# Optimization experiments

Measured on AMD Instinct MI355X. Metric: run time of the kernel, lower is better.

## Reference

```python
import jax, jax.numpy as jnp
import numpy as np

PAST = 12
FUTURE = 12


def setup_inputs() -> dict:
    key = jax.random.key(0)
    k1, k2, k3, k4, k5 = jax.random.split(key, 5)
    B, L, D = 64, 256, 512
    inp = jax.random.normal(k1, (B, L, D), dtype=jnp.float32)
    W_t = jax.random.normal(k2, (FUTURE, PAST), dtype=jnp.float32) / np.sqrt(PAST)
    b_t = jax.random.normal(k3, (FUTURE,), dtype=jnp.float32) * 0.01
    W_s = jax.random.normal(k4, (D, D), dtype=jnp.float32) / np.sqrt(D)
    b_s = jax.random.normal(k5, (D,), dtype=jnp.float32) * 0.01
    return {"inp": inp, "W_t": W_t, "b_t": b_t, "W_s": W_s, "b_s": b_s}


def reference(inp, W_t, b_t, W_s, b_s):
    # inp: [B, L, D]. Sliding windows of size PAST -> W = L - PAST windows.
    B, L, D = inp.shape
    W = L - PAST
    # gather windows: [B, W, PAST, D]
    idx = jnp.arange(W)[:, None] + jnp.arange(PAST)[None, :]  # [W, PAST]
    x_win = inp[:, idx, :]  # [B, W, PAST, D]
    # temporal Linear(PAST -> FUTURE) along window-time axis
    t = jnp.einsum('bwpd,fp->bwfd', x_win, W_t) + b_t[None, None, :, None]
    # spatial Linear(D -> D) along last axis
    out = jnp.einsum('bwfd,ed->bwfe', t, W_s) + b_s
    return out  # [B, W, FUTURE, D]
```

## Files before the change

kernel.cpp:

```cpp
#include <hip/hip_runtime.h>

#define PAST 12
#define FUTURE 12
#define NB 64
#define NL 256
#define ND 512
#define NW 244

typedef unsigned short ushort_t;
typedef __attribute__((ext_vector_type(8))) short short8;
typedef __attribute__((ext_vector_type(4))) float floatx4;

__device__ inline unsigned int f2bf(float x) {
    unsigned int u = __float_as_uint(x);
    return (u + 0x7fffu + ((u >> 16) & 1u)) >> 16;
}

__global__ __launch_bounds__(256) void prep_ws(
    const float* __restrict__ Ws, ushort_t* __restrict__ Wsb, float* __restrict__ S)
{
    const int row = blockIdx.x;
    const int t = threadIdx.x;
    const float2 v = *(const float2*)(Ws + (size_t)row * ND + t * 2);
    *(unsigned int*)(Wsb + (size_t)row * ND + t * 2) = f2bf(v.x) | (f2bf(v.y) << 16);
    float s = v.x + v.y;
#pragma unroll
    for (int o = 32; o > 0; o >>= 1) s += __shfl_down(s, o);
    __shared__ float red[4];
    if ((t & 63) == 0) red[t >> 6] = s;
    __syncthreads();
    if (t == 0) S[row] = red[0] + red[1] + red[2] + red[3];
}

#define BM 128
#define BN 128
#define BK 32

#define STAGE_A_LOAD(k0) do { \
    _Pragma("unroll") \
    for (int c = 0; c < 4; ++c) av[c] = *(const float4*)(aptr[c] + (k0)); \
} while (0)

#define STAGE_A_WRITE(dst) do { \
    _Pragma("unroll") \
    for (int c = 0; c < 4; ++c) { \
        uint2 o; \
        o.x = f2bf(av[c].x) | (f2bf(av[c].y) << 16); \
        o.y = f2bf(av[c].z) | (f2bf(av[c].w) << 16); \
        *(uint2*)((dst) + tid * 4 + c * 1024) = o; \
    } \
} while (0)

#define STAGE_B(k0, dst) do { \
    _Pragma("unroll") \
    for (int r = 0; r < 2; ++r) { \
        const ushort_t* gb = Bm + (size_t)(n0 + (tid >> 2) + r * 64) * ND + (k0) + (tid & 3) * 8; \
        __builtin_amdgcn_global_load_lds( \
            (const __attribute__((address_space(1))) unsigned int*)gb, \
            (__attribute__((address_space(3))) unsigned int*)((dst) + r * 2048 + tid * 8), \
            16, 0, 0); \
    } \
} while (0)

#define GEMM_STEP(cura, curb) do { \
    const ushort_t* a_base = (cura) + (wm + (lane & 15)) * BK + (lane >> 4) * 8; \
    const ushort_t* b_base = (curb) + (wn + (lane & 15)) * BK + (lane >> 4) * 8; \
    short8 af[4], bq[4]; \
    _Pragma("unroll") \
    for (int t = 0; t < 4; ++t) { \
        af[t] = *(const short8*)(a_base + t * 16 * BK); \
        bq[t] = *(const short8*)(b_base + t * 16 * BK); \
    } \
    _Pragma("unroll") \
    for (int i = 0; i < 4; ++i) \
    _Pragma("unroll") \
    for (int j = 0; j < 4; ++j) \
        acc[i][j] = __builtin_amdgcn_mfma_f32_16x16x32_bf16(af[i], bq[j], acc[i][j], 0, 0, 0); \
} while (0)

#define FULL_STEP(k, cura, curb, nxta, nxtb) do { \
    if ((k) < 15) { STAGE_A_LOAD(((k) + 1) * BK); STAGE_B(((k) + 1) * BK, nxtb); } \
    GEMM_STEP(cura, curb); \
    if ((k) < 15) STAGE_A_WRITE(nxta); \
    __syncthreads(); \
} while (0)

__global__ __launch_bounds__(256) void gemm_spatial(
    const float* __restrict__ A,
    const ushort_t* __restrict__ Bm,
    ushort_t* __restrict__ Y)
{
    __shared__ __align__(16) ushort_t As0[BM * BK];
    __shared__ __align__(16) ushort_t As1[BM * BK];
    __shared__ __align__(16) ushort_t Bs0[BN * BK];
    __shared__ __align__(16) ushort_t Bs1[BN * BK];

    const int tid  = threadIdx.x;
    const int wave = tid >> 6;
    const int lane = tid & 63;
    const int m0 = blockIdx.y * BM;
    const int n0 = blockIdx.x * BN;
    const int wm = (wave >> 1) * 64;
    const int wn = (wave & 1) * 64;

    floatx4 acc[4][4] = {};

    const float* aptr[4];
#pragma unroll
    for (int c = 0; c < 4; ++c) {
        const int i = c * 256 + tid;
        aptr[c] = A + (size_t)(m0 + (i >> 3)) * ND + (i & 7) * 4;
    }

    float4 av[4];

    STAGE_A_LOAD(0);
    STAGE_B(0, Bs0);
    STAGE_A_WRITE(As0);
    __syncthreads();

    for (int k = 0; k < 16; k += 2) {
        FULL_STEP(k,     As0, Bs0, As1, Bs1);
        FULL_STEP(k + 1, As1, Bs1, As0, Bs0);
    }

#pragma unroll
    for (int i = 0; i < 4; ++i) {
        const int m_base = m0 + wm + i * 16 + (lane >> 4) * 4;
#pragma unroll
        for (int j = 0; j < 4; ++j) {
            const int n = n0 + wn + j * 16 + (lane & 15);
#pragma unroll
            for (int r = 0; r < 4; ++r) {
                Y[(size_t)(m_base + r) * ND + n] = (ushort_t)f2bf(acc[i][j][r]);
            }
        }
    }
}

#define WTILE 8

__global__ __launch_bounds__(256) void temporal_kernel(
    const ushort_t* __restrict__ Y,
    const float*    __restrict__ Wt,
    const float*    __restrict__ bt,
    const float*    __restrict__ bs,
    const float*    __restrict__ S,
    float*          __restrict__ Out)
{
    const int tid = threadIdx.x;
    const int b  = blockIdx.y;
    const int w0 = blockIdx.x * WTILE + (tid >> 7) * 4;
    const int eq = (tid & 127) * 4;

    const float4 Sv  = *(const float4*)(S + eq);
    const float4 bsv = *(const float4*)(bs + eq);

    float win[PAST + 3][4];
    const ushort_t* ybase = Y + ((size_t)(b * NL + w0)) * ND + eq;
#pragma unroll
    for (int i = 0; i < PAST + 3; ++i) {
        if (w0 + i < NL) {
            const uint2 v = *(const uint2*)(ybase + (size_t)i * ND);
            win[i][0] = __uint_as_float(v.x << 16);
            win[i][1] = __uint_as_float(v.x & 0xffff0000u);
            win[i][2] = __uint_as_float(v.y << 16);
            win[i][3] = __uint_as_float(v.y & 0xffff0000u);
        } else {
            win[i][0] = win[i][1] = win[i][2] = win[i][3] = 0.f;
        }
    }

#pragma unroll
    for (int w = 0; w < 4; ++w) {
        if (w0 + w < NW) {
            float* orow = Out + ((size_t)(b * NW + (w0 + w)) * FUTURE) * ND + eq;
#pragma unroll
            for (int f = 0; f < FUTURE; ++f) {
                const float btf = bt[f];
                float a0 = fmaf(btf, Sv.x, bsv.x);
                float a1 = fmaf(btf, Sv.y, bsv.y);
                float a2 = fmaf(btf, Sv.z, bsv.z);
                float a3 = fmaf(btf, Sv.w, bsv.w);
#pragma unroll
                for (int p = 0; p < PAST; ++p) {
                    const float c = Wt[f * PAST + p];
                    a0 = fmaf(c, win[w + p][0], a0);
                    a1 = fmaf(c, win[w + p][1], a1);
                    a2 = fmaf(c, win[w + p][2], a2);
                    a3 = fmaf(c, win[w + p][3], a3);
                }
                *(float4*)(orow + (size_t)f * ND) = make_float4(a0, a1, a2, a3);
            }
        }
    }
}

extern "C" void kernel_launch(void* const* d_in, const int* in_sizes, int n_in,
                              void* d_out, int out_size, void* d_ws, size_t ws_size,
                              hipStream_t stream) {
    const float* inp = (const float*)d_in[0];
    const float* Wt  = (const float*)d_in[1];
    const float* bt  = (const float*)d_in[2];
    const float* Ws  = (const float*)d_in[3];
    const float* bs  = (const float*)d_in[4];
    float* out = (float*)d_out;

    const size_t n_inp = (size_t)NB * NL * ND;
    ushort_t* Y    = (ushort_t*)d_ws;
    ushort_t* Ws_b = (ushort_t*)((char*)d_ws + n_inp * 2);
    float*    S    = (float*)((char*)d_ws + n_inp * 2 + (size_t)ND * ND * 2);

    prep_ws<<<dim3(ND), dim3(256), 0, stream>>>(Ws, Ws_b, S);
    gemm_spatial<<<dim3(ND / BN, (NB * NL) / BM), dim3(256), 0, stream>>>(inp, Ws_b, Y);
    temporal_kernel<<<dim3((NW + WTILE - 1) / WTILE, NB), dim3(256), 0, stream>>>(Y, Wt, bt, bs, S, out);
}
```

Baseline: 437.6 us.

## Shrink GEMM M-tile, remap blocks across XCDs, and use nontemporal output stores

The spatial GEMM tile height drops from 128 to 64 rows, which doubles the block count and halves accumulator registers. The A staging is simplified to one row segment per thread. Both the GEMM and the temporal kernel switch to 1D grids with an XCD-aware remap (bid&7 striding), so neighbouring tiles land on the same chiplet and share L2. The large output writes use nontemporal stores to avoid polluting cache. The trade-off is more redundant B-tile loads per output element in exchange for better occupancy and locality.

```diff
diff --git a/kernel.cpp b/kernel.cpp
--- a/kernel.cpp
+++ b/kernel.cpp
@@ -32,23 +32,22 @@
     if (t == 0) S[row] = red[0] + red[1] + red[2] + red[3];
 }
 
-#define BM 128
+#define BM 64
 #define BN 128
 #define BK 32
 
 #define STAGE_A_LOAD(k0) do { \
-    _Pragma("unroll") \
-    for (int c = 0; c < 4; ++c) av[c] = *(const float4*)(aptr[c] + (k0)); \
+    av0 = *(const float4*)(aptr + (k0)); \
+    av1 = *(const float4*)(aptr + (k0) + 4); \
 } while (0)
 
 #define STAGE_A_WRITE(dst) do { \
-    _Pragma("unroll") \
-    for (int c = 0; c < 4; ++c) { \
-        uint2 o; \
-        o.x = f2bf(av[c].x) | (f2bf(av[c].y) << 16); \
-        o.y = f2bf(av[c].z) | (f2bf(av[c].w) << 16); \
-        *(uint2*)((dst) + tid * 4 + c * 1024) = o; \
-    } \
+    uint4 o; \
+    o.x = f2bf(av0.x) | (f2bf(av0.y) << 16); \
+    o.y = f2bf(av0.z) | (f2bf(av0.w) << 16); \
+    o.z = f2bf(av1.x) | (f2bf(av1.y) << 16); \
+    o.w = f2bf(av1.z) | (f2bf(av1.w) << 16); \
+    *(uint4*)((dst) + tid * 8) = o; \
 } while (0)
 
 #define STAGE_B(k0, dst) do { \
@@ -65,14 +64,13 @@
 #define GEMM_STEP(cura, curb) do { \
     const ushort_t* a_base = (cura) + (wm + (lane & 15)) * BK + (lane >> 4) * 8; \
     const ushort_t* b_base = (curb) + (wn + (lane & 15)) * BK + (lane >> 4) * 8; \
-    short8 af[4], bq[4]; \
-    _Pragma("unroll") \
-    for (int t = 0; t < 4; ++t) { \
-        af[t] = *(const short8*)(a_base + t * 16 * BK); \
-        bq[t] = *(const short8*)(b_base + t * 16 * BK); \
-    } \
-    _Pragma("unroll") \
-    for (int i = 0; i < 4; ++i) \
+    short8 af[2], bq[4]; \
+    _Pragma("unroll") \
+    for (int t = 0; t < 2; ++t) af[t] = *(const short8*)(a_base + t * 16 * BK); \
+    _Pragma("unroll") \
+    for (int t = 0; t < 4; ++t) bq[t] = *(const short8*)(b_base + t * 16 * BK); \
+    _Pragma("unroll") \
+    for (int i = 0; i < 2; ++i) \
     _Pragma("unroll") \
     for (int j = 0; j < 4; ++j) \
         acc[i][j] = __builtin_amdgcn_mfma_f32_16x16x32_bf16(af[i], bq[j], acc[i][j], 0, 0, 0); \
@@ -98,21 +96,18 @@
     const int tid  = threadIdx.x;
     const int wave = tid >> 6;
     const int lane = tid & 63;
-    const int m0 = blockIdx.y * BM;
-    const int n0 = blockIdx.x * BN;
-    const int wm = (wave >> 1) * 64;
+
+    const int bid = blockIdx.x;
+    const int idx = (bid & 7) * 128 + (bid >> 3);
+    const int n0 = (idx & 3) * BN;
+    const int m0 = (idx >> 2) * BM;
+    const int wm = (wave >> 1) * 32;
     const int wn = (wave & 1) * 64;
 
-    floatx4 acc[4][4] = {};
-
-    const float* aptr[4];
-#pragma unroll
-    for (int c = 0; c < 4; ++c) {
-        const int i = c * 256 + tid;
-        aptr[c] = A + (size_t)(m0 + (i >> 3)) * ND + (i & 7) * 4;
-    }
-
-    float4 av[4];
+    floatx4 acc[2][4] = {};
+
+    const float* aptr = A + (size_t)(m0 + (tid >> 2)) * ND + (tid & 3) * 8;
+    float4 av0, av1;
 
     STAGE_A_LOAD(0);
     STAGE_B(0, Bs0);
@@ -125,7 +120,7 @@
     }
 
 #pragma unroll
-    for (int i = 0; i < 4; ++i) {
+    for (int i = 0; i < 2; ++i) {
         const int m_base = m0 + wm + i * 16 + (lane >> 4) * 4;
 #pragma unroll
         for (int j = 0; j < 4; ++j) {
@@ -139,6 +134,7 @@
 }
 
 #define WTILE 8
+#define TGRID (((NW + WTILE - 1) / WTILE) * NB)
 
 __global__ __launch_bounds__(256) void temporal_kernel(
     const ushort_t* __restrict__ Y,
@@ -149,8 +145,11 @@
     float*          __restrict__ Out)
 {
     const int tid = threadIdx.x;
-    const int b  = blockIdx.y;
-    const int w0 = blockIdx.x * WTILE + (tid >> 7) * 4;
+    const int bid = blockIdx.x;
+    const int idx = (bid & 7) * (TGRID / 8) + (bid >> 3);
+    const int b   = idx / 31;
+    const int wx  = idx % 31;
+    const int w0 = wx * WTILE + (tid >> 7) * 4;
     const int eq = (tid & 127) * 4;
 
     const float4 Sv  = *(const float4*)(S + eq);
@@ -190,7 +189,9 @@
                     a2 = fmaf(c, win[w + p][2], a2);
                     a3 = fmaf(c, win[w + p][3], a3);
                 }
-                *(float4*)(orow + (size_t)f * ND) = make_float4(a0, a1, a2, a3);
+                floatx4 ov;
+                ov.x = a0; ov.y = a1; ov.z = a2; ov.w = a3;
+                __builtin_nontemporal_store(ov, (floatx4*)(orow + (size_t)f * ND));
             }
         }
     }
@@ -212,6 +213,6 @@
     float*    S    = (float*)((char*)d_ws + n_inp * 2 + (size_t)ND * ND * 2);
 
     prep_ws<<<dim3(ND), dim3(256), 0, stream>>>(Ws, Ws_b, S);
-    gemm_spatial<<<dim3(ND / BN, (NB * NL) / BM), dim3(256), 0, stream>>>(inp, Ws_b, Y);
-    temporal_kernel<<<dim3((NW + WTILE - 1) / WTILE, NB), dim3(256), 0, stream>>>(Y, Wt, bt, bs, S, out);
-}
+    gemm_spatial<<<dim3((NB * NL / BM) * (ND / BN)), dim3(256), 0, stream>>>(inp, Ws_b, Y);
+    temporal_kernel<<<dim3(TGRID), dim3(256), 0, stream>>>(Y, Wt, bt, bs, S, out);
+}
```

Result: no change. 431.3 us (-1.5%).
